# Performance work log

Hardware: AMD Instinct MI355X
Metric: run time of the kernel (lower is better)

Reference implementation:

```python
import jax, jax.numpy as jnp
import numpy as np

N_NODES = 100000
N_EDGES = 1600000
IN_DIM = 128
OUT_DIM = 128


def setup_inputs() -> dict:
    key = jax.random.key(0)
    k1, k2, k3, k4, k5 = jax.random.split(key, 5)
    features = jax.random.normal(k1, (N_NODES, IN_DIM), dtype=jnp.float32)
    # Xavier-uniform-ish init for the dense transform weight
    limit = float(np.sqrt(6.0 / (IN_DIM + OUT_DIM)))
    weight = jax.random.uniform(k2, (IN_DIM, OUT_DIM), dtype=jnp.float32,
                                minval=-limit, maxval=limit)
    bias = jnp.zeros((OUT_DIM,), dtype=jnp.float32)
    # Sparse adjacency in COO form: edge i contributes
    # edge_weight[i] * support[src[i]] into output row dst[i].
    edge_weight = jax.random.uniform(k3, (N_EDGES,), dtype=jnp.float32)
    src = jax.random.randint(k4, (N_EDGES,), 0, N_NODES)
    dst = jax.random.randint(k5, (N_EDGES,), 0, N_NODES)
    return {"features": features, "weight": weight, "bias": bias,
            "edge_weight": edge_weight, "src": src, "dst": dst}


def reference(features, weight, bias, edge_weight, src, dst):
    # support = X @ W  (dense GEMM: [N, in] x [in, out])
    support = features @ weight
    # output = A @ support, with A sparse in COO form -> gather + scatter-add
    msgs = support[src] * edge_weight[:, None]          # [E, out]
    out = jax.ops.segment_sum(msgs, dst, num_segments=features.shape[0])
    return out + bias
```

## Files before the change

kernel.cpp:

```cpp
#include <hip/hip_runtime.h>
#include <hip/hip_bf16.h>

#define DIM 128
#define EPB 4096
#define SRC_BITS 17
#define SRC_MASK 0x1FFFF
#define TMAX 8
#define CAP 4864

typedef short short8 __attribute__((ext_vector_type(8)));
typedef float f32x4 __attribute__((ext_vector_type(4)));

static __device__ __forceinline__ unsigned short f2bf(float f) {
    unsigned u = __builtin_bit_cast(unsigned, f);
    unsigned r = (u + 0x7fffu + ((u >> 16) & 1u)) >> 16;
    return (unsigned short)r;
}

__global__ __launch_bounds__(256) void gemm_xw_mfma(const float* __restrict__ X,
                                                    const float* __restrict__ W,
                                                    unsigned short* __restrict__ S2,
                                                    int* __restrict__ cursor,
                                                    int n_nodes) {
    __shared__ unsigned short wlds[DIM * DIM];

    if (blockIdx.x == 0) {
        for (int i = threadIdx.x; i < 512; i += 256) cursor[i * 16] = 0;
    }

    for (int idx = threadIdx.x; idx < DIM * DIM; idx += 256) {
        const int k = idx >> 7;
        const int n = idx & 127;
        wlds[n * DIM + (k ^ ((n & 7) << 3))] = f2bf(W[idx]);
    }
    __syncthreads();

    const int wave = threadIdx.x >> 6;
    const int lane = threadIdx.x & 63;
    const int row_base = blockIdx.x * 64 + wave * 16;
    const int mrow = lane & 15;
    const int kq = lane >> 4;
    const int kq8 = kq * 8;

    int rr = row_base + mrow;
    if (rr >= n_nodes) rr = n_nodes - 1;
    const float4* Xr = (const float4*)(X + (size_t)rr * DIM);

    short8 a[4];
#pragma unroll
    for (int s = 0; s < 4; ++s) {
        const float4 v0 = Xr[s * 8 + kq * 2];
        const float4 v1 = Xr[s * 8 + kq * 2 + 1];
        short8 av;
        av[0] = f2bf(v0.x); av[1] = f2bf(v0.y); av[2] = f2bf(v0.z); av[3] = f2bf(v0.w);
        av[4] = f2bf(v1.x); av[5] = f2bf(v1.y); av[6] = f2bf(v1.z); av[7] = f2bf(v1.w);
        a[s] = av;
    }

    f32x4 acc[8];
#pragma unroll
    for (int c = 0; c < 8; ++c) acc[c] = (f32x4){0.f, 0.f, 0.f, 0.f};

    const int swz = (lane & 7) << 3;
#pragma unroll
    for (int s = 0; s < 4; ++s) {
        const int k0 = s * 32 + kq8;
#pragma unroll
        for (int c = 0; c < 8; ++c) {
            const int n = c * 16 + mrow;
            const short8 bv = *(const short8*)(&wlds[n * DIM + (k0 ^ swz)]);
            acc[c] = __builtin_amdgcn_mfma_f32_16x16x32_bf16(a[s], bv, acc[c], 0, 0, 0);
        }
    }

#pragma unroll
    for (int reg = 0; reg < 4; ++reg) {
        const int g_r = row_base + kq * 4 + reg;
        if (g_r < n_nodes) {
            unsigned short* orow = S2 + (size_t)g_r * DIM + mrow;
#pragma unroll
            for (int c = 0; c < 8; ++c) orow[c * 16] = f2bf(acc[c][reg]);
        }
    }
}

__global__ __launch_bounds__(1024) void partB_scatter(const int* __restrict__ dst,
                                                      const int* __restrict__ src,
                                                      const float* __restrict__ ew,
                                                      int* __restrict__ cursor,
                                                      int2* __restrict__ part_sw,
                                                      int n_edges, int nbkt) {
    __shared__ int lc[512];
    __shared__ int lbase[512];
    const int blk = blockIdx.x;
    for (int i = threadIdx.x; i < 512; i += 1024) lc[i] = 0;
    __syncthreads();

    const int base = blk * EPB;
    int d[4], rk[4];
#pragma unroll
    for (int u = 0; u < 4; ++u) {
        const int e = base + u * 1024 + threadIdx.x;
        if (e < n_edges) {
            d[u] = dst[e];
            rk[u] = atomicAdd(&lc[d[u] >> 8], 1);
        }
    }
    __syncthreads();

    for (int b = threadIdx.x; b < nbkt; b += 1024)
        lbase[b] = (lc[b] > 0) ? atomicAdd(&cursor[b * 16], lc[b]) : 0;
    __syncthreads();

#pragma unroll
    for (int u = 0; u < 4; ++u) {
        const int e = base + u * 1024 + threadIdx.x;
        if (e < n_edges) {
            const int bin = d[u] >> 8;
            const int pos = bin * CAP + lbase[bin] + rk[u];
            part_sw[pos] = make_int2(src[e] | ((d[u] & 255) << SRC_BITS),
                                     __float_as_int(ew[e]));
        }
    }
}

__global__ __launch_bounds__(1024) void partC_csr(const int2* __restrict__ part_sw,
                                                  const int* __restrict__ cursor,
                                                  int2* __restrict__ offs2,
                                                  int2* __restrict__ edge_sw,
                                                  int n_nodes) {
    __shared__ int lcnt[256];
    __shared__ int loff[256];
    const int b = blockIdx.x;
    const int bstart = b * CAP;
    const int bcount = cursor[b * 16];

    if (threadIdx.x < 256) lcnt[threadIdx.x] = 0;
    __syncthreads();

    int2 sw_r[TMAX];
    int rk_r[TMAX];
    const int ntile = (bcount + 1023) >> 10;
#pragma unroll
    for (int t = 0; t < TMAX; ++t) {
        if (t < ntile) {
            const int i = t * 1024 + threadIdx.x;
            if (i < bcount) {
                const int2 v = part_sw[bstart + i];
                sw_r[t] = v;
                rk_r[t] = atomicAdd(&lcnt[(v.x >> SRC_BITS) & 255], 1);
            }
        }
    }
    __syncthreads();

    if (threadIdx.x < 256) loff[threadIdx.x] = lcnt[threadIdx.x];
    __syncthreads();
#pragma unroll
    for (int off = 1; off < 256; off <<= 1) {
        int t_ = 0;
        if (threadIdx.x < 256 && threadIdx.x >= off) t_ = loff[threadIdx.x - off];
        __syncthreads();
        if (threadIdx.x < 256) loff[threadIdx.x] += t_;
        __syncthreads();
    }
    int ex = 0;
    if (threadIdx.x < 256 && threadIdx.x > 0) ex = loff[threadIdx.x - 1];
    __syncthreads();
    if (threadIdx.x < 256) loff[threadIdx.x] = ex;
    __syncthreads();

    const int nb0 = b << 8;
    if (threadIdx.x < 256 && nb0 + threadIdx.x < n_nodes) {
        const int s = bstart + loff[threadIdx.x];
        offs2[nb0 + threadIdx.x] = make_int2(s, s + lcnt[threadIdx.x]);
    }

#pragma unroll
    for (int t = 0; t < TMAX; ++t) {
        if (t < ntile) {
            const int i = t * 1024 + threadIdx.x;
            if (i < bcount) {
                const int ld = (sw_r[t].x >> SRC_BITS) & 255;
                edge_sw[bstart + loff[ld] + rk_r[t]] =
                    make_int2(sw_r[t].x & SRC_MASK, sw_r[t].y);
            }
        }
    }
}

#define QEXPAND(GV, WW)                                                   \
    acc[0] = fmaf(WW, __int_as_float((GV).x << 16), acc[0]);              \
    acc[1] = fmaf(WW, __int_as_float((GV).x & 0xffff0000u), acc[1]);      \
    acc[2] = fmaf(WW, __int_as_float((GV).y << 16), acc[2]);              \
    acc[3] = fmaf(WW, __int_as_float((GV).y & 0xffff0000u), acc[3]);      \
    acc[4] = fmaf(WW, __int_as_float((GV).z << 16), acc[4]);              \
    acc[5] = fmaf(WW, __int_as_float((GV).z & 0xffff0000u), acc[5]);      \
    acc[6] = fmaf(WW, __int_as_float((GV).w << 16), acc[6]);              \
    acc[7] = fmaf(WW, __int_as_float((GV).w & 0xffff0000u), acc[7]);

__global__ __launch_bounds__(256) void gcn_reduce(const uint4* __restrict__ S2q,
                                                  const int2* __restrict__ edge_sw,
                                                  const int2* __restrict__ offs2,
                                                  const float* __restrict__ bias,
                                                  float* __restrict__ out,
                                                  int n_nodes) {
    const int node = blockIdx.x * 4 + (threadIdx.x >> 6);
    if (node >= n_nodes) return;
    const int lane = threadIdx.x & 63;
    const int grp = lane >> 4;
    const int ql = lane & 15;

    const int2 se = offs2[node];
    const int start = se.x;
    const int end = se.y;

    float acc[8];
#pragma unroll
    for (int j = 0; j < 8; ++j) acc[j] = 0.f;

    for (int base = start; base < end; base += 64) {
        const int cnt = min(64, end - base);
        int2 meta = make_int2(0, 0);
        if (lane < cnt) meta = edge_sw[base + lane];

        int i = 0;
        for (; i + 16 <= cnt; i += 16) {
            uint4 gv[4];
            float ws[4];
#pragma unroll
            for (int u = 0; u < 4; ++u) {
                const int idx = i + u * 4 + grp;
                const int s = __shfl(meta.x, idx, 64);
                ws[u] = __int_as_float(__shfl(meta.y, idx, 64));
                gv[u] = S2q[(size_t)s * 16 + ql];
            }
            QEXPAND(gv[0], ws[0]);
            QEXPAND(gv[1], ws[1]);
            QEXPAND(gv[2], ws[2]);
            QEXPAND(gv[3], ws[3]);
        }
        for (; i < cnt; i += 4) {
            const int idx = i + grp;
            const int s = __shfl(meta.x, idx, 64);
            const float w = __int_as_float(__shfl(meta.y, idx, 64));
            const uint4 gv = S2q[(size_t)s * 16 + ql];
            QEXPAND(gv, w);
        }
    }

#pragma unroll
    for (int j = 0; j < 8; ++j) {
        acc[j] += __shfl_xor(acc[j], 16, 64);
        acc[j] += __shfl_xor(acc[j], 32, 64);
    }

    if (lane < 16) {
        const float4 b0 = ((const float4*)bias)[ql * 2];
        const float4 b1 = ((const float4*)bias)[ql * 2 + 1];
        float4 o0 = {acc[0] + b0.x, acc[1] + b0.y, acc[2] + b0.z, acc[3] + b0.w};
        float4 o1 = {acc[4] + b1.x, acc[5] + b1.y, acc[6] + b1.z, acc[7] + b1.w};
        float4* orow = (float4*)(out + (size_t)node * DIM) + ql * 2;
        orow[0] = o0;
        orow[1] = o1;
    }
}

extern "C" void kernel_launch(void* const* d_in, const int* in_sizes, int n_in,
                              void* d_out, int out_size, void* d_ws, size_t ws_size,
                              hipStream_t stream) {
    const float* X    = (const float*)d_in[0];
    const float* W    = (const float*)d_in[1];
    const float* bias = (const float*)d_in[2];
    const float* ew   = (const float*)d_in[3];
    const int*   src  = (const int*)d_in[4];
    const int*   dst  = (const int*)d_in[5];
    float* out = (float*)d_out;

    const int n_nodes = in_sizes[0] / DIM;
    const int n_edges = in_sizes[3];

    const int nbkt = (n_nodes + 255) >> 8;
    const int nchunks = (n_edges + EPB - 1) / EPB;

    char* ws = (char*)d_ws;
    unsigned short* S2 = (unsigned short*)ws;
    char* p = ws + (size_t)n_nodes * DIM * 2;
    int* cursor = (int*)p;          p += 512 * 16 * 4;
    int2* offs2 = (int2*)p;         p += (size_t)n_nodes * 8;
    int2* part_sw = (int2*)p;       p += (size_t)nbkt * CAP * 8;
    int2* edge_sw = (int2*)p;

    gemm_xw_mfma<<<(n_nodes + 63) / 64, 256, 0, stream>>>(X, W, S2, cursor, n_nodes);

    partB_scatter<<<nchunks, 1024, 0, stream>>>(dst, src, ew, cursor, part_sw,
                                                n_edges, nbkt);

    partC_csr<<<nbkt, 1024, 0, stream>>>(part_sw, cursor, offs2, edge_sw, n_nodes);

    gcn_reduce<<<(n_nodes + 3) / 4, 256, 0, stream>>>((const uint4*)S2,
                                                      edge_sw, offs2,
                                                      bias, out, n_nodes);
}
```

Measured before the change: 124.5 us.

## Fuse GEMM and edge bucketing into one launch with block-range dispatch

Merges the dense X@W GEMM and the edge bucket-scatter kernel into a single launch: the first nchunks blocks do edge partitioning (now 256 threads, 16 edges each, reusing the weight LDS buffer for counters) and the rest do the GEMM. This lets the memory-bound scatter overlap with the MFMA GEMM and removes one dependent launch boundary. Cursor zeroing moves to a separate tiny kernel, since the fused kernel can no longer reset it safely itself. The risks are an extra launch, higher register pressure from the 16-element arrays, and a shared-memory footprint sized for the GEMM that may limit occupancy of the scatter blocks.

```diff
diff --git a/kernel.cpp b/kernel.cpp
--- a/kernel.cpp
+++ b/kernel.cpp
@@ -17,15 +17,55 @@
     return (unsigned short)r;
 }
 
-__global__ __launch_bounds__(256) void gemm_xw_mfma(const float* __restrict__ X,
-                                                    const float* __restrict__ W,
-                                                    unsigned short* __restrict__ S2,
-                                                    int* __restrict__ cursor,
-                                                    int n_nodes) {
+__global__ void zero_cursor(int* __restrict__ cursor) {
+    cursor[threadIdx.x * 16] = 0;
+}
+
+__global__ __launch_bounds__(256) void gemm_partB(const float* __restrict__ X,
+                                                  const float* __restrict__ W,
+                                                  unsigned short* __restrict__ S2,
+                                                  const int* __restrict__ dst,
+                                                  const int* __restrict__ src,
+                                                  const float* __restrict__ ew,
+                                                  int* __restrict__ cursor,
+                                                  int2* __restrict__ part_sw,
+                                                  int n_nodes, int n_edges,
+                                                  int nchunks, int nbkt) {
     __shared__ unsigned short wlds[DIM * DIM];
 
-    if (blockIdx.x == 0) {
-        for (int i = threadIdx.x; i < 512; i += 256) cursor[i * 16] = 0;
+    if (blockIdx.x < nchunks) {
+        int* lc = (int*)wlds;
+        int* lbase = lc + 512;
+        for (int i = threadIdx.x; i < 512; i += 256) lc[i] = 0;
+        __syncthreads();
+
+        const int base = blockIdx.x * EPB;
+        int d[16], rk[16];
+#pragma unroll
+        for (int u = 0; u < 16; ++u) {
+            const int e = base + u * 256 + threadIdx.x;
+            if (e < n_edges) {
+                d[u] = dst[e];
+                rk[u] = atomicAdd(&lc[d[u] >> 8], 1);
+            }
+        }
+        __syncthreads();
+
+        for (int b = threadIdx.x; b < nbkt; b += 256)
+            lbase[b] = (lc[b] > 0) ? atomicAdd(&cursor[b * 16], lc[b]) : 0;
+        __syncthreads();
+
+#pragma unroll
+        for (int u = 0; u < 16; ++u) {
+            const int e = base + u * 256 + threadIdx.x;
+            if (e < n_edges) {
+                const int bin = d[u] >> 8;
+                const int pos = bin * CAP + lbase[bin] + rk[u];
+                part_sw[pos] = make_int2(src[e] | ((d[u] & 255) << SRC_BITS),
+                                         __float_as_int(ew[e]));
+            }
+        }
+        return;
     }
 
     for (int idx = threadIdx.x; idx < DIM * DIM; idx += 256) {
@@ -35,9 +75,10 @@
     }
     __syncthreads();
 
+    const int bid = blockIdx.x - nchunks;
     const int wave = threadIdx.x >> 6;
     const int lane = threadIdx.x & 63;
-    const int row_base = blockIdx.x * 64 + wave * 16;
+    const int row_base = bid * 64 + wave * 16;
     const int mrow = lane & 15;
     const int kq = lane >> 4;
     const int kq8 = kq * 8;
@@ -80,46 +121,6 @@
             unsigned short* orow = S2 + (size_t)g_r * DIM + mrow;
 #pragma unroll
             for (int c = 0; c < 8; ++c) orow[c * 16] = f2bf(acc[c][reg]);
-        }
-    }
-}
-
-__global__ __launch_bounds__(1024) void partB_scatter(const int* __restrict__ dst,
-                                                      const int* __restrict__ src,
-                                                      const float* __restrict__ ew,
-                                                      int* __restrict__ cursor,
-                                                      int2* __restrict__ part_sw,
-                                                      int n_edges, int nbkt) {
-    __shared__ int lc[512];
-    __shared__ int lbase[512];
-    const int blk = blockIdx.x;
-    for (int i = threadIdx.x; i < 512; i += 1024) lc[i] = 0;
-    __syncthreads();
-
-    const int base = blk * EPB;
-    int d[4], rk[4];
-#pragma unroll
-    for (int u = 0; u < 4; ++u) {
-        const int e = base + u * 1024 + threadIdx.x;
-        if (e < n_edges) {
-            d[u] = dst[e];
-            rk[u] = atomicAdd(&lc[d[u] >> 8], 1);
-        }
-    }
-    __syncthreads();
-
-    for (int b = threadIdx.x; b < nbkt; b += 1024)
-        lbase[b] = (lc[b] > 0) ? atomicAdd(&cursor[b * 16], lc[b]) : 0;
-    __syncthreads();
-
-#pragma unroll
-    for (int u = 0; u < 4; ++u) {
-        const int e = base + u * 1024 + threadIdx.x;
-        if (e < n_edges) {
-            const int bin = d[u] >> 8;
-            const int pos = bin * CAP + lbase[bin] + rk[u];
-            part_sw[pos] = make_int2(src[e] | ((d[u] & 255) << SRC_BITS),
-                                     __float_as_int(ew[e]));
         }
     }
 }
@@ -282,6 +283,7 @@
 
     const int nbkt = (n_nodes + 255) >> 8;
     const int nchunks = (n_edges + EPB - 1) / EPB;
+    const int gemmB = (n_nodes + 63) / 64;
 
     char* ws = (char*)d_ws;
     unsigned short* S2 = (unsigned short*)ws;
@@ -291,10 +293,12 @@
     int2* part_sw = (int2*)p;       p += (size_t)nbkt * CAP * 8;
     int2* edge_sw = (int2*)p;
 
-    gemm_xw_mfma<<<(n_nodes + 63) / 64, 256, 0, stream>>>(X, W, S2, cursor, n_nodes);
-
-    partB_scatter<<<nchunks, 1024, 0, stream>>>(dst, src, ew, cursor, part_sw,
-                                                n_edges, nbkt);
+    zero_cursor<<<1, 512, 0, stream>>>(cursor);
+
+    gemm_partB<<<nchunks + gemmB, 256, 0, stream>>>(X, W, S2, dst, src, ew,
+                                                    cursor, part_sw,
+                                                    n_nodes, n_edges,
+                                                    nchunks, nbkt);
 
     partC_csr<<<nbkt, 1024, 0, stream>>>(part_sw, cursor, offs2, edge_sw, n_nodes);
 
```

Result: no change. 126.8 us (+1.8%).
